# Kernel tuning notes

Hardware: AMD Instinct MI355X
Metric: run time of the kernel (lower is better)

## Reference

```python
import jax, jax.numpy as jnp
import numpy as np

B, I, H = 16384, 1024, 1024

def setup_inputs() -> dict:
    key = jax.random.key(0)
    ks = jax.random.split(key, 7)
    scale = 0.02  # small init so gates are not saturated
    return {
        "x": jax.random.normal(ks[0], (B, I), jnp.float32),
        "h_prev": jax.random.normal(ks[1], (B, H), jnp.float32),
        "c_prev": jax.random.normal(ks[2], (B, H), jnp.float32),
        "Wx": jax.random.normal(ks[3], (4, H, I), jnp.float32) * scale,  # order: z,i,f,o
        "bx": jnp.zeros((4, H), jnp.float32),
        "Rh": jax.random.normal(ks[4], (4, H, H), jnp.float32) * scale,
        "bh": jnp.zeros((4, H), jnp.float32),
    }

def reference(x, h_prev, c_prev, Wx, bx, Rh, bh):
    # Fused form of 4 input-GEMMs + 4 recurrent-GEMMs: two einsums over stacked gates.
    # gate order g=0..3 -> z, i, f, o
    pre = (jnp.einsum('bi,ghi->bgh', x, Wx) + bx[None]
           + jnp.einsum('bh,gkh->bgk', h_prev, Rh) + bh[None])  # [B,4,H]
    z = jnp.tanh(pre[:, 0])
    i = jax.nn.sigmoid(pre[:, 1])
    f = jax.nn.sigmoid(pre[:, 2])
    o = jax.nn.sigmoid(pre[:, 3])
    c = f * c_prev + i * z
    h = o * jnp.tanh(c)
    return (h, c)
```

## Files before the change

### kernel.cpp

```cpp
#include <hip/hip_runtime.h>
#include <hip/hip_bf16.h>
#include <stdint.h>


typedef __attribute__((ext_vector_type(8))) short bf16x8;
typedef __attribute__((ext_vector_type(4))) float f32x4;
typedef __attribute__((ext_vector_type(8))) unsigned short u16x8;

#define AS1 __attribute__((address_space(1)))
#define AS3 __attribute__((address_space(3)))

constexpr int BATCH = 16384;
constexpr int HDIM  = 1024;
constexpr int KDIM  = 2048;
constexpr int NDIM  = 4096;

__device__ inline unsigned short f2bf(float f) {
  uint32_t u = __builtin_bit_cast(uint32_t, f);
  u += 0x7fffu + ((u >> 16) & 1u);
  return (unsigned short)(u >> 16);
}
__device__ inline u16x8 cvt8(const float* __restrict__ src) {
  float4 f0 = *(const float4*)src;
  float4 f1 = *(const float4*)(src + 4);
  u16x8 v;
  v[0] = f2bf(f0.x); v[1] = f2bf(f0.y); v[2] = f2bf(f0.z); v[3] = f2bf(f0.w);
  v[4] = f2bf(f1.x); v[5] = f2bf(f1.y); v[6] = f2bf(f1.z); v[7] = f2bf(f1.w);
  return v;
}
__device__ inline float sigmoid_f(float x) {
  float e = __builtin_amdgcn_exp2f(-1.4426950408889634f * x);
  return __builtin_amdgcn_rcpf(1.0f + e);
}
__device__ inline float tanh_f(float x) {
  float e = __builtin_amdgcn_exp2f(2.8853900817779268f * x);
  return 1.0f - 2.0f * __builtin_amdgcn_rcpf(1.0f + e);
}

__global__ void pack_xh(const float* __restrict__ x, const float* __restrict__ hp,
                        unsigned short* __restrict__ xh) {
  const int64_t nch = (int64_t)BATCH * KDIM / 8;
  for (int64_t c = (int64_t)blockIdx.x * blockDim.x + threadIdx.x; c < nch;
       c += (int64_t)gridDim.x * blockDim.x) {
    const int b = (int)(c >> 8);
    const int k = ((int)c & 255) * 8;
    const float* src = (k < 1024) ? (x + (int64_t)b * 1024 + k)
                                  : (hp + (int64_t)b * 1024 + (k - 1024));
    *(u16x8*)(xh + c * 8) = cvt8(src);
  }
}
__global__ void pack_w(const float* __restrict__ Wx, const float* __restrict__ Rh,
                       unsigned short* __restrict__ wp) {
  const int64_t nch = (int64_t)NDIM * KDIM / 8;
  for (int64_t c = (int64_t)blockIdx.x * blockDim.x + threadIdx.x; c < nch;
       c += (int64_t)gridDim.x * blockDim.x) {
    const int np = (int)(c >> 8);
    const int k = ((int)c & 255) * 8;
    const int h = np >> 2, g = np & 3;
    const float* src = (k < 1024) ? (Wx + (int64_t)(g * HDIM + h) * 1024 + k)
                                  : (Rh + (int64_t)(g * HDIM + h) * 1024 + (k - 1024));
    *(u16x8*)(wp + c * 8) = cvt8(src);
  }
}
__global__ void pack_bias(const float* __restrict__ bx, const float* __restrict__ bh,
                          float* __restrict__ bias) {
  int n = blockIdx.x * blockDim.x + threadIdx.x;
  if (n < NDIM) {
    int h = n >> 2, g = n & 3;
    bias[n] = bx[g * HDIM + h] + bh[g * HDIM + h];
  }
}

template <int OFF>
__device__ __forceinline__ bf16x8 dsb128(uint32_t a) {
  bf16x8 r;
  asm volatile("ds_read_b128 %0, %1 offset:%2" : "=v"(r) : "v"(a), "i"(OFF) : "memory");
  return r;
}

#define BARR   asm volatile("s_barrier" ::: "memory")
#define LGKM4  asm volatile("s_waitcnt lgkmcnt(4)" ::: "memory")
#define LGKM8  asm volatile("s_waitcnt lgkmcnt(8)" ::: "memory")
#define VM6    asm volatile("s_waitcnt vmcnt(6)" ::: "memory")
#define VM0    asm volatile("s_waitcnt vmcnt(0)" ::: "memory")
#define SCHED0 __builtin_amdgcn_sched_barrier(0)

#define ISS_A(FA, BUF, KH, MH) { constexpr int _o = (BUF)*32768 + (KH)*16384 + (MH)*4096; \
  FA[0] = dsb128<_o>(av); FA[1] = dsb128<_o+1024>(av);                                     \
  FA[2] = dsb128<_o+2048>(av); FA[3] = dsb128<_o+3072>(av); }
#define ISS_B(FB, BUF, KH) { constexpr int _o = (BUF)*32768 + (KH)*16384; \
  FB[0] = dsb128<_o>(bv); FB[1] = dsb128<_o+1024>(bv);                     \
  FB[2] = dsb128<_o+2048>(bv); FB[3] = dsb128<_o+3072>(bv); }

#define MFMA16(FA, FB, MB) { \
  __builtin_amdgcn_s_setprio(1); \
  _Pragma("unroll") for (int j = 0; j < 4; ++j) \
  _Pragma("unroll") for (int ni = 0; ni < 4; ++ni) \
    acc[(MB)*4 + j][ni] = __builtin_amdgcn_mfma_f32_16x16x32_bf16(FA[j], FB[ni], acc[(MB)*4 + j][ni], 0, 0, 0); \
  __builtin_amdgcn_s_setprio(0); }

#define STAGE(SRC, DOFF) { \
  __builtin_amdgcn_global_load_lds((const AS1 void*)(SRC), (AS3 void*)(dstL + (DOFF)), 16, 0, 0); \
  __builtin_amdgcn_global_load_lds((const AS1 void*)((SRC) + 524288), (AS3 void*)(dstL + (DOFF) + 8192), 16, 0, 0); }

__global__ __launch_bounds__(512, 2) void lstm_gemm(
    const unsigned short* __restrict__ XH, const unsigned short* __restrict__ Wp,
    const float* __restrict__ bias, const float* __restrict__ c_prev,
    float* __restrict__ out_h, float* __restrict__ out_c) {
  __shared__ __align__(1024) char smem_[131072];

  const int tid  = threadIdx.x;
  const int l    = tid & 63;
  const int w    = tid >> 6;
  const int wr   = w >> 2, wc = w & 3;
  const int la   = l & 15;
  const int kg   = l >> 4;

  const int xcd = blockIdx.x & 7;
  const int q   = blockIdx.x >> 3;
  const int tn  = xcd * 2 + (q & 1);
  const int tm  = q >> 1;
  const int m0  = tm * 256;
  const int n0  = tn * 256;

  const int rbase = w * 16 + (l >> 2);
  const int ck    = (l & 3) ^ ((l >> 3) & 3);
  const char* pA = (const char*)XH + (int64_t)(m0 + rbase) * 4096 + ck * 16;
  const char* pB = (const char*)Wp + (int64_t)(n0 + rbase) * 4096 + ck * 16;
  char* dstL = smem_ + w * 1024;

  const int cc = kg ^ ((la >> 1) & 3);
  const uint32_t lds0 = (uint32_t)(uintptr_t)(AS3 char*)smem_;
  const uint32_t av = lds0 + wr * 8192 + la * 64 + cc * 16;
  const uint32_t bv = lds0 + 65536 + wc * 4096 + la * 64 + cc * 16;

  f32x4 acc[8][4] = {};
  bf16x8 fa0[4], fa1[4], fb0[4], fb1[4];

  STAGE(pB,       65536);
  STAGE(pA,       0);
  STAGE(pB + 64,  81920);
  STAGE(pA + 64,  16384);
  STAGE(pB + 128, 98304);
  STAGE(pA + 128, 32768);
  STAGE(pB + 192, 114688);
  VM6; BARR;
  ISS_B(fb0, 0, 0) ISS_A(fa0, 0, 0, 0)

#pragma unroll 1
  for (int it = 0; it < 16; ++it) {
    int kt2 = 2 * it + 2; if (kt2 > 31) kt2 = 31;
    int kt3 = 2 * it + 3; if (kt3 > 31) kt3 = 31;
    const char* sA1 = pA + (2 * it + 1) * 128;
    const char* sA2 = pA + kt2 * 128;
    const char* sA3 = pA + kt3 * 128;
    const char* sB2 = pB + kt2 * 128;
    const char* sB3 = pB + kt3 * 128;

    BARR;
    STAGE(sA1 + 64, 49152);
    ISS_A(fa1, 0, 0, 1)
    LGKM4; SCHED0; MFMA16(fa0, fb0, 0)
    BARR;
    STAGE(sB2, 65536);
    ISS_B(fb1, 0, 1) ISS_A(fa0, 0, 1, 0)
    LGKM8; SCHED0; MFMA16(fa1, fb0, 1)
    VM6;
    BARR;
    STAGE(sA2, 0);
    ISS_A(fa1, 0, 1, 1)
    LGKM4; SCHED0; MFMA16(fa0, fb1, 0)
    BARR;
    STAGE(sB2 + 64, 81920);
    ISS_B(fb0, 1, 0) ISS_A(fa0, 1, 0, 0)
    LGKM8; SCHED0; MFMA16(fa1, fb1, 1)
    VM6;
    BARR;
    STAGE(sA2 + 64, 16384);
    ISS_A(fa1, 1, 0, 1)
    LGKM4; SCHED0; MFMA16(fa0, fb0, 0)
    BARR;
    STAGE(sB3, 98304);
    ISS_B(fb1, 1, 1) ISS_A(fa0, 1, 1, 0)
    LGKM8; SCHED0; MFMA16(fa1, fb0, 1)
    VM6;
    BARR;
    STAGE(sA3, 32768);
    ISS_A(fa1, 1, 1, 1)
    LGKM4; SCHED0; MFMA16(fa0, fb1, 0)
    BARR;
    STAGE(sB3 + 64, 114688);
    ISS_B(fb0, 0, 0) ISS_A(fa0, 0, 0, 0)
    LGKM8; SCHED0; MFMA16(fa1, fb1, 1)
    VM6;
  }

  VM0;
  __syncthreads();
  float* ew = (float*)smem_ + w * 1088;
  const float4 bias4 = *(const float4*)(bias + n0 + wc * 64 + 4 * la);
  const int hg = ((n0 + wc * 64) >> 2) + la;

#pragma unroll
  for (int mi = 0; mi < 8; ++mi) {
#pragma unroll
    for (int ni = 0; ni < 4; ++ni)
#pragma unroll
      for (int r = 0; r < 4; ++r)
        ew[(4 * kg + r) * 68 + ni * 16 + la] = acc[mi][ni][r];
#pragma unroll
    for (int p = 0; p < 4; ++p) {
      const int row = p * 4 + kg;
      float4 g4 = *(const float4*)(ew + row * 68 + 4 * la);
      const int b = m0 + wr * 128 + mi * 16 + row;
      const uint32_t oidx = (uint32_t)b * HDIM + (uint32_t)hg;
      const float cp = c_prev[oidx];
      const float zg = tanh_f(g4.x + bias4.x);
      const float ig = sigmoid_f(g4.y + bias4.y);
      const float fg = sigmoid_f(g4.z + bias4.z);
      const float og = sigmoid_f(g4.w + bias4.w);
      const float cn = fg * cp + ig * zg;
      out_h[oidx] = og * tanh_f(cn);
      out_c[oidx] = cn;
    }
  }
}

extern "C" void kernel_launch(void* const* d_in, const int* in_sizes, int n_in,
                              void* d_out, int out_size, void* d_ws, size_t ws_size,
                              hipStream_t stream) {
  const float* x  = (const float*)d_in[0];
  const float* hp = (const float*)d_in[1];
  const float* cp = (const float*)d_in[2];
  const float* Wx = (const float*)d_in[3];
  const float* bx = (const float*)d_in[4];
  const float* Rh = (const float*)d_in[5];
  const float* bh = (const float*)d_in[6];

  unsigned short* XH = (unsigned short*)d_ws;
  unsigned short* Wp = XH + (size_t)BATCH * KDIM;
  float* bias = (float*)(Wp + (size_t)NDIM * KDIM);
  float* out_h = (float*)d_out;
  float* out_c = out_h + (size_t)BATCH * HDIM;

  pack_xh<<<2048, 256, 0, stream>>>(x, hp, XH);
  pack_w<<<1024, 256, 0, stream>>>(Wx, Rh, Wp);
  pack_bias<<<16, 256, 0, stream>>>(bx, bh, bias);
  lstm_gemm<<<1024, 512, 0, stream>>>(XH, Wp, bias, cp, out_h, out_c);
}
```

Baseline: 306.5 us.

## Switch GEMM inner tile from 16x16x32 to 32x32x16 bf16 MFMA

```diff
diff --git a/kernel.cpp b/kernel.cpp
--- a/kernel.cpp
+++ b/kernel.cpp
@@ -4,7 +4,7 @@
 
 
 typedef __attribute__((ext_vector_type(8))) short bf16x8;
-typedef __attribute__((ext_vector_type(4))) float f32x4;
+typedef __attribute__((ext_vector_type(16))) float f32x16;
 typedef __attribute__((ext_vector_type(8))) unsigned short u16x8;
 
 #define AS1 __attribute__((address_space(1)))
@@ -85,18 +85,23 @@
 #define VM0    asm volatile("s_waitcnt vmcnt(0)" ::: "memory")
 #define SCHED0 __builtin_amdgcn_sched_barrier(0)
 
-#define ISS_A(FA, BUF, KH, MH) { constexpr int _o = (BUF)*32768 + (KH)*16384 + (MH)*4096; \
-  FA[0] = dsb128<_o>(av); FA[1] = dsb128<_o+1024>(av);                                     \
-  FA[2] = dsb128<_o+2048>(av); FA[3] = dsb128<_o+3072>(av); }
+#define ISS_A(FA, BUF, KH, MBH) { constexpr int _o = (BUF)*32768 + (KH)*16384 + (MBH)*4096; \
+  FA[0] = dsb128<_o>(av0);      FA[1] = dsb128<_o>(av1);                                     \
+  FA[2] = dsb128<_o+2048>(av0); FA[3] = dsb128<_o+2048>(av1); }
 #define ISS_B(FB, BUF, KH) { constexpr int _o = (BUF)*32768 + (KH)*16384; \
-  FB[0] = dsb128<_o>(bv); FB[1] = dsb128<_o+1024>(bv);                     \
-  FB[2] = dsb128<_o+2048>(bv); FB[3] = dsb128<_o+3072>(bv); }
-
-#define MFMA16(FA, FB, MB) { \
+  FB[0] = dsb128<_o>(bv0);      FB[1] = dsb128<_o>(bv1);                   \
+  FB[2] = dsb128<_o+2048>(bv0); FB[3] = dsb128<_o+2048>(bv1); }
+
+#define MFMA8(FA, FB, MBH) { \
   __builtin_amdgcn_s_setprio(1); \
-  _Pragma("unroll") for (int j = 0; j < 4; ++j) \
-  _Pragma("unroll") for (int ni = 0; ni < 4; ++ni) \
-    acc[(MB)*4 + j][ni] = __builtin_amdgcn_mfma_f32_16x16x32_bf16(FA[j], FB[ni], acc[(MB)*4 + j][ni], 0, 0, 0); \
+  acc[(MBH)*2+0][0] = __builtin_amdgcn_mfma_f32_32x32x16_bf16(FA[0], FB[0], acc[(MBH)*2+0][0], 0, 0, 0); \
+  acc[(MBH)*2+0][1] = __builtin_amdgcn_mfma_f32_32x32x16_bf16(FA[0], FB[2], acc[(MBH)*2+0][1], 0, 0, 0); \
+  acc[(MBH)*2+1][0] = __builtin_amdgcn_mfma_f32_32x32x16_bf16(FA[2], FB[0], acc[(MBH)*2+1][0], 0, 0, 0); \
+  acc[(MBH)*2+1][1] = __builtin_amdgcn_mfma_f32_32x32x16_bf16(FA[2], FB[2], acc[(MBH)*2+1][1], 0, 0, 0); \
+  acc[(MBH)*2+0][0] = __builtin_amdgcn_mfma_f32_32x32x16_bf16(FA[1], FB[1], acc[(MBH)*2+0][0], 0, 0, 0); \
+  acc[(MBH)*2+0][1] = __builtin_amdgcn_mfma_f32_32x32x16_bf16(FA[1], FB[3], acc[(MBH)*2+0][1], 0, 0, 0); \
+  acc[(MBH)*2+1][0] = __builtin_amdgcn_mfma_f32_32x32x16_bf16(FA[3], FB[1], acc[(MBH)*2+1][0], 0, 0, 0); \
+  acc[(MBH)*2+1][1] = __builtin_amdgcn_mfma_f32_32x32x16_bf16(FA[3], FB[3], acc[(MBH)*2+1][1], 0, 0, 0); \
   __builtin_amdgcn_s_setprio(0); }
 
 #define STAGE(SRC, DOFF) { \
@@ -113,8 +118,6 @@
   const int l    = tid & 63;
   const int w    = tid >> 6;
   const int wr   = w >> 2, wc = w & 3;
-  const int la   = l & 15;
-  const int kg   = l >> 4;
 
   const int xcd = blockIdx.x & 7;
   const int q   = blockIdx.x >> 3;
@@ -129,12 +132,16 @@
   const char* pB = (const char*)Wp + (int64_t)(n0 + rbase) * 4096 + ck * 16;
   char* dstL = smem_ + w * 1024;
 
-  const int cc = kg ^ ((la >> 1) & 3);
+  const int r5  = l & 31;
+  const int kh5 = l >> 5;
+  const int qa0 = kh5 ^ ((r5 >> 1) & 3);
   const uint32_t lds0 = (uint32_t)(uintptr_t)(AS3 char*)smem_;
-  const uint32_t av = lds0 + wr * 8192 + la * 64 + cc * 16;
-  const uint32_t bv = lds0 + 65536 + wc * 4096 + la * 64 + cc * 16;
-
-  f32x4 acc[8][4] = {};
+  const uint32_t av0 = lds0 + wr * 8192 + r5 * 64 + qa0 * 16;
+  const uint32_t av1 = av0 ^ 32;
+  const uint32_t bv0 = lds0 + 65536 + wc * 4096 + r5 * 64 + qa0 * 16;
+  const uint32_t bv1 = bv0 ^ 32;
+
+  f32x16 acc[4][2] = {};
   bf16x8 fa0[4], fa1[4], fb0[4], fb1[4];
 
   STAGE(pB,       65536);
@@ -160,59 +167,59 @@
     BARR;
     STAGE(sA1 + 64, 49152);
     ISS_A(fa1, 0, 0, 1)
-    LGKM4; SCHED0; MFMA16(fa0, fb0, 0)
+    LGKM4; SCHED0; MFMA8(fa0, fb0, 0)
     BARR;
     STAGE(sB2, 65536);
     ISS_B(fb1, 0, 1) ISS_A(fa0, 0, 1, 0)
-    LGKM8; SCHED0; MFMA16(fa1, fb0, 1)
+    LGKM8; SCHED0; MFMA8(fa1, fb0, 1)
     VM6;
     BARR;
     STAGE(sA2, 0);
     ISS_A(fa1, 0, 1, 1)
-    LGKM4; SCHED0; MFMA16(fa0, fb1, 0)
+    LGKM4; SCHED0; MFMA8(fa0, fb1, 0)
     BARR;
     STAGE(sB2 + 64, 81920);
     ISS_B(fb0, 1, 0) ISS_A(fa0, 1, 0, 0)
-    LGKM8; SCHED0; MFMA16(fa1, fb1, 1)
+    LGKM8; SCHED0; MFMA8(fa1, fb1, 1)
     VM6;
     BARR;
     STAGE(sA2 + 64, 16384);
     ISS_A(fa1, 1, 0, 1)
-    LGKM4; SCHED0; MFMA16(fa0, fb0, 0)
+    LGKM4; SCHED0; MFMA8(fa0, fb0, 0)
     BARR;
     STAGE(sB3, 98304);
     ISS_B(fb1, 1, 1) ISS_A(fa0, 1, 1, 0)
-    LGKM8; SCHED0; MFMA16(fa1, fb0, 1)
+    LGKM8; SCHED0; MFMA8(fa1, fb0, 1)
     VM6;
     BARR;
     STAGE(sA3, 32768);
     ISS_A(fa1, 1, 1, 1)
-    LGKM4; SCHED0; MFMA16(fa0, fb1, 0)
+    LGKM4; SCHED0; MFMA8(fa0, fb1, 0)
     BARR;
     STAGE(sB3 + 64, 114688);
     ISS_B(fb0, 0, 0) ISS_A(fa0, 0, 0, 0)
-    LGKM8; SCHED0; MFMA16(fa1, fb1, 1)
+    LGKM8; SCHED0; MFMA8(fa1, fb1, 1)
     VM6;
   }
 
   VM0;
   __syncthreads();
-  float* ew = (float*)smem_ + w * 1088;
-  const float4 bias4 = *(const float4*)(bias + n0 + wc * 64 + 4 * la);
-  const int hg = ((n0 + wc * 64) >> 2) + la;
-
-#pragma unroll
-  for (int mi = 0; mi < 8; ++mi) {
-#pragma unroll
-    for (int ni = 0; ni < 4; ++ni)
-#pragma unroll
-      for (int r = 0; r < 4; ++r)
-        ew[(4 * kg + r) * 68 + ni * 16 + la] = acc[mi][ni][r];
-#pragma unroll
-    for (int p = 0; p < 4; ++p) {
-      const int row = p * 4 + kg;
-      float4 g4 = *(const float4*)(ew + row * 68 + 4 * la);
-      const int b = m0 + wr * 128 + mi * 16 + row;
+  float* ew = (float*)smem_ + w * 2176;
+  const float4 bias4 = *(const float4*)(bias + n0 + wc * 64 + 4 * (l & 15));
+  const int hg = ((n0 + wc * 64) >> 2) + (l & 15);
+
+#pragma unroll
+  for (int mb = 0; mb < 4; ++mb) {
+#pragma unroll
+    for (int nb = 0; nb < 2; ++nb)
+#pragma unroll
+      for (int r = 0; r < 16; ++r)
+        ew[((r & 3) + 8 * (r >> 2) + 4 * kh5) * 68 + nb * 32 + r5] = acc[mb][nb][r];
+#pragma unroll
+    for (int p = 0; p < 8; ++p) {
+      const int row = p * 4 + (l >> 4);
+      float4 g4 = *(const float4*)(ew + row * 68 + 4 * (l & 15));
+      const int b = m0 + wr * 128 + mb * 32 + row;
       const uint32_t oidx = (uint32_t)b * HDIM + (uint32_t)hg;
       const float cp = c_prev[oidx];
       const float zg = tanh_f(g4.x + bias4.x);
```

Result: slower. 329.3 us (+7.4%).
